# Kernel optimization log

Measured on AMD Instinct MI355X. Metric: run time of the kernel, lower is better.

The kernel has to match this reference:

```python
import math
import jax, jax.numpy as jnp
import numpy as np

EPS = 1e-6
MAX_SCALE_LOG = math.log(100.0)

def rms_norm(x, scale, eps=EPS):
    # x * scale / rms(x), reduction over last dim
    ms = jnp.mean(jnp.square(x), axis=-1, keepdims=True)
    return x * (scale * jax.lax.rsqrt(ms + eps))

def axial_rope_theta(pos, n_heads, d_head, dtype):
    # freqs: linspace in log-space from pi to 10*pi, reshaped to [n_heads, d_head//4]
    f = np.exp(np.linspace(math.log(math.pi), math.log(10.0 * math.pi),
                           n_heads * d_head // 4 + 1)[:-1])
    freqs = jnp.asarray(f.reshape(d_head // 4, n_heads).T, dtype)  # [h, e/4]
    theta_h = pos[:, :, None, 0:1] * freqs  # [n, l, h, e/4]
    theta_w = pos[:, :, None, 1:2] * freqs  # [n, l, h, e/4]
    theta = jnp.concatenate([theta_h, theta_w], axis=-1)  # [n, l, h, e/2]
    return theta.transpose(0, 2, 1, 3)  # [n, h, l, e/2]

def apply_rotary(x, theta):
    d = theta.shape[-1]
    x1, x2, x3 = x[..., :d], x[..., d:2 * d], x[..., 2 * d:]
    cos, sin = jnp.cos(theta), jnp.sin(theta)
    return jnp.concatenate([x1 * cos - x2 * sin, x2 * cos + x1 * sin, x3], axis=-1)

def setup_inputs() -> dict:
    key = jax.random.key(0)
    ks = jax.random.split(key, 8)
    n, l, d_model, d_head = 2, 2048, 1024, 64
    n_heads = d_model // d_head
    x = jax.random.normal(ks[0], (n, l, d_model), jnp.float32)
    pos = jax.random.uniform(ks[1], (n, l, 2), jnp.float32)
    cond = jax.random.normal(ks[2], (n, 1, d_model), jnp.float32)
    # params (torch uses zero-init for w_cond/w_out; small random for a non-degenerate baseline)
    w_cond = jax.random.normal(ks[3], (d_model, d_model), jnp.float32) * 0.02
    w_qkv = jax.random.normal(ks[4], (d_model, 3 * d_model), jnp.float32) * (d_model ** -0.5)
    qk_scale = jnp.full((n_heads,), math.log(10.0), jnp.float32)
    w_out = jax.random.normal(ks[5], (d_model, d_model), jnp.float32) * 0.02
    return {"x": x, "pos": pos, "cond": cond, "w_cond": w_cond,
            "w_qkv": w_qkv, "qk_scale": qk_scale, "w_out": w_out}

def reference(x, pos, cond, w_cond, w_qkv, qk_scale, w_out):
    n, l, d_model = x.shape
    h = qk_scale.shape[0]
    e = d_model // h
    # AdaRMSNorm: scale = linear(cond) + 1
    xn = rms_norm(x, cond @ w_cond + 1.0)
    # QKV projection
    q, k, v = jnp.split(xn @ w_qkv, 3, axis=-1)
    to_heads = lambda t: t.reshape(n, l, h, e).transpose(0, 2, 1, 3)  # [n,h,l,e]
    q, k, v = to_heads(q), to_heads(k), to_heads(v)
    # QKNorm: per-head learned scale, rms over head dim
    s = jnp.exp(0.5 * jnp.minimum(qk_scale, MAX_SCALE_LOG) - 0.25 * math.log(e))
    q = rms_norm(q, s[:, None, None])
    k = rms_norm(k, s[:, None, None])
    # Axial RoPE
    theta = axial_rope_theta(pos, h, e, x.dtype)
    q = apply_rotary(q, theta)
    k = apply_rotary(k, theta)
    # SDPA (no mask)
    attn = jax.nn.softmax(jnp.einsum('nhqe,nhke->nhqk', q, k) / math.sqrt(e), axis=-1)
    o = jnp.einsum('nhqk,nhke->nhqe', attn, v)
    o = o.transpose(0, 2, 1, 3).reshape(n, l, d_model)
    return o @ w_out
```

## Files before the change

kernel.cpp:

```cpp
#include <hip/hip_runtime.h>

typedef unsigned short u16;
typedef unsigned int u32;
typedef short s16x8 __attribute__((ext_vector_type(8)));
typedef short s16x4 __attribute__((ext_vector_type(4)));
typedef float f32x4 __attribute__((ext_vector_type(4)));
typedef float f32x16 __attribute__((ext_vector_type(16)));

#define AS1 __attribute__((address_space(1)))
#define AS3 __attribute__((address_space(3)))

__device__ __forceinline__ float bf2f(u16 u) {
    union { unsigned int i; float f; } x; x.i = ((unsigned int)u) << 16; return x.f;
}
__device__ __forceinline__ u16 f2bf(float f) {
    union { float f; unsigned int i; } x; x.f = f;
    unsigned int r = (x.i + 0x7FFFu + ((x.i >> 16) & 1u)) >> 16;
    return (u16)r;
}
__device__ __forceinline__ void storeOut(u16* p, float v) { *p = f2bf(v); }
__device__ __forceinline__ void storeOut(float* p, float v) { *p = v; }
__device__ __forceinline__ float loadIn(const void* p, size_t i, int isf32) {
    return isf32 ? ((const float*)p)[i] : bf2f(((const u16*)p)[i]);
}
__device__ __forceinline__ float fexp2(float x) {
#if __has_builtin(__builtin_amdgcn_exp2f)
    return __builtin_amdgcn_exp2f(x);
#else
    return exp2f(x);
#endif
}
__device__ __forceinline__ void plswap(u32& a, u32& b) {
#if __has_builtin(__builtin_amdgcn_permlane32_swap)
    const auto r = __builtin_amdgcn_permlane32_swap(a, b, false, false);
    a = (u32)r[0]; b = (u32)r[1];
#else
    asm("v_permlane32_swap_b32 %0, %1" : "+v"(a), "+v"(b));
#endif
}

__global__ __launch_bounds__(256) void detect_dtype(const u16* __restrict__ x,
                                                    int* __restrict__ flag) {
    __shared__ int cnt[4];
    const int tid = threadIdx.x;
    int c = 0;
    #pragma unroll
    for (int i = 0; i < 4; ++i) {
        const u16 u = x[tid * 4 + i];
        const int e = (u >> 7) & 0xFF;
        c += (e >= 101 && e <= 135) ? 1 : 0;
    }
    #pragma unroll
    for (int m = 1; m < 64; m <<= 1) c += __shfl_xor(c, m, 64);
    if ((tid & 63) == 0) cnt[tid >> 6] = c;
    __syncthreads();
    if (tid == 0) {
        const int t = cnt[0] + cnt[1] + cnt[2] + cnt[3];
        *flag = (t < 800) ? 1 : 0;
    }
}

__global__ __launch_bounds__(256) void cond_gemv(const void* __restrict__ cond,
                                                 const void* __restrict__ w,
                                                 float* __restrict__ out,
                                                 const int* __restrict__ flag) {
    const int isf32 = *flag;
    const int d  = blockIdx.x * 256 + threadIdx.x;
    const int n  = blockIdx.y;
    const int k0 = blockIdx.z * 64;
    float acc = 0.f;
    #pragma unroll 8
    for (int k = 0; k < 64; ++k)
        acc += loadIn(cond, n * 1024 + k0 + k, isf32) *
               loadIn(w, (size_t)(k0 + k) * 1024 + d, isf32);
    atomicAdd(out + n * 1024 + d, acc);
}

__global__ __launch_bounds__(256) void rmsnorm_x(const void* __restrict__ x,
                                                 const float* __restrict__ scl,
                                                 u16* __restrict__ xn,
                                                 const int* __restrict__ flag) {
    const int isf32 = *flag;
    const int tok = blockIdx.x;
    const int n = tok >> 11;
    u16* orow = xn + (size_t)tok * 1024;
    const int base = threadIdx.x * 4;
    float f0, f1, f2, f3;
    if (isf32) {
        const float4 v = *(const float4*)((const float*)x + (size_t)tok * 1024 + base);
        f0 = v.x; f1 = v.y; f2 = v.z; f3 = v.w;
    } else {
        s16x4 uv = *(const s16x4*)((const u16*)x + (size_t)tok * 1024 + base);
        f0 = bf2f((u16)uv[0]); f1 = bf2f((u16)uv[1]); f2 = bf2f((u16)uv[2]); f3 = bf2f((u16)uv[3]);
    }
    float ss = f0 * f0 + f1 * f1 + f2 * f2 + f3 * f3;
    #pragma unroll
    for (int m = 1; m < 64; m <<= 1) ss += __shfl_xor(ss, m, 64);
    __shared__ float red[4];
    const int wave = threadIdx.x >> 6, lane = threadIdx.x & 63;
    if (lane == 0) red[wave] = ss;
    __syncthreads();
    float ms = (red[0] + red[1] + red[2] + red[3]) * (1.f / 1024.f);
    float rinv = rsqrtf(ms + 1e-6f);
    orow[base + 0] = f2bf(f0 * (scl[n * 1024 + base + 0] + 1.f) * rinv);
    orow[base + 1] = f2bf(f1 * (scl[n * 1024 + base + 1] + 1.f) * rinv);
    orow[base + 2] = f2bf(f2 * (scl[n * 1024 + base + 2] + 1.f) * rinv);
    orow[base + 3] = f2bf(f3 * (scl[n * 1024 + base + 3] + 1.f) * rinv);
}

__global__ __launch_bounds__(256) void transpose_bf(const void* __restrict__ src,
                                                    u16* __restrict__ dst, int R, int C,
                                                    const int* __restrict__ flag) {
    const int isf32 = *flag;
    __shared__ u16 t[32][33];
    const int c0 = blockIdx.x * 32, r0 = blockIdx.y * 32;
    const int tx = threadIdx.x & 31, ty = threadIdx.x >> 5;
    #pragma unroll
    for (int i = 0; i < 4; ++i)
        t[ty + i * 8][tx] = f2bf(loadIn(src, (size_t)(r0 + ty + i * 8) * C + c0 + tx, isf32));
    __syncthreads();
    #pragma unroll
    for (int i = 0; i < 4; ++i)
        dst[(size_t)(c0 + ty + i * 8) * R + r0 + tx] = t[tx][ty + i * 8];
}

template <typename OutT>
__global__ __launch_bounds__(256) void gemm_bt(const u16* __restrict__ A,
                                               const u16* __restrict__ BT,
                                               OutT* __restrict__ C, int Nn, int K) {
    __shared__ u16 As[128 * 32];
    __shared__ u16 Bs[128 * 32];
    const int tid = threadIdx.x;
    const int wave = tid >> 6, lane = tid & 63;
    const int l15 = lane & 15, quad = lane >> 4;
    const int bm0 = blockIdx.y * 128, bn0 = blockIdx.x * 128;
    const int wr = wave >> 1, wc = wave & 1;
    f32x4 acc[4][4] = {};
    const int srow = lane >> 2;
    const int g = (lane & 3) ^ (srow & 3);
    for (int bk = 0; bk < K; bk += 32) {
        __syncthreads();
        #pragma unroll
        for (int p = 0; p < 2; ++p) {
            const int rowl = p * 64 + wave * 16 + srow;
            const u16* ga = A + (size_t)(bm0 + rowl) * K + bk + g * 8;
            u16* la = As + (p * 64 + wave * 16) * 32;
            __builtin_amdgcn_global_load_lds((const AS1 void*)ga, (AS3 void*)la, 16, 0, 0);
            const u16* gb = BT + (size_t)(bn0 + rowl) * K + bk + g * 8;
            u16* lb = Bs + (p * 64 + wave * 16) * 32;
            __builtin_amdgcn_global_load_lds((const AS1 void*)gb, (AS3 void*)lb, 16, 0, 0);
        }
        __syncthreads();
        s16x8 af[4], bfr[4];
        #pragma unroll
        for (int mt = 0; mt < 4; ++mt) {
            const int r = wr * 64 + mt * 16 + l15;
            af[mt] = *(const s16x8*)(As + r * 32 + ((quad ^ (r & 3)) << 3));
        }
        #pragma unroll
        for (int nt = 0; nt < 4; ++nt) {
            const int r = wc * 64 + nt * 16 + l15;
            bfr[nt] = *(const s16x8*)(Bs + r * 32 + ((quad ^ (r & 3)) << 3));
        }
        #pragma unroll
        for (int mt = 0; mt < 4; ++mt)
            #pragma unroll
            for (int nt = 0; nt < 4; ++nt)
                acc[mt][nt] = __builtin_amdgcn_mfma_f32_16x16x32_bf16(af[mt], bfr[nt], acc[mt][nt], 0, 0, 0);
    }
    #pragma unroll
    for (int mt = 0; mt < 4; ++mt)
        #pragma unroll
        for (int nt = 0; nt < 4; ++nt)
            #pragma unroll
            for (int r = 0; r < 4; ++r) {
                const int row = bm0 + wr * 64 + mt * 16 + quad * 4 + r;
                const int col = bn0 + wc * 64 + nt * 16 + l15;
                storeOut(C + (size_t)row * Nn + col, acc[mt][nt][r]);
            }
}

__global__ __launch_bounds__(256) void qkv_head(const u16* __restrict__ qkv,
                                                const void* __restrict__ pos,
                                                const void* __restrict__ qk_scale,
                                                u16* __restrict__ q_ws,
                                                u16* __restrict__ k_ws,
                                                u16* __restrict__ vtg,
                                                const int* __restrict__ flag) {
    const int isf32 = *flag;
    const int nh = blockIdx.y;
    const int n = nh >> 4, h = nh & 15;
    const int l0 = blockIdx.x * 64;
    const int tid = threadIdx.x;
    const int wave = tid >> 6, lane = tid & 63;

    const float qs = loadIn(qk_scale, h, isf32);
    const float s = __expf(0.5f * fminf(qs, 4.605170186f) - 1.039720771f);
    const float qmul = s * s * 0.125f * 1.44269504089f;
    const int j = lane & 31;
    const float t = (float)((j & 15) * 16 + h);
    const float freq = 3.14159265358979f * __expf(t * (2.302585093f / 256.f));
    const int pj = j >> 4;

    #pragma unroll 2
    for (int it = 0; it < 16; ++it) {
        const int l = l0 + wave * 16 + it;
        const int tok = n * 2048 + l;
        const u16* row = qkv + (size_t)tok * 3072;
        float qv = bf2f(row[h * 64 + lane]);
        float kv = bf2f(row[1024 + h * 64 + lane]);
        float q2 = qv * qv, k2 = kv * kv;
        #pragma unroll
        for (int m = 1; m < 64; m <<= 1) { q2 += __shfl_xor(q2, m, 64); k2 += __shfl_xor(k2, m, 64); }
        float qn = qv * rsqrtf(q2 * (1.f / 64.f) + 1e-6f) * qmul;
        float kn = kv * rsqrtf(k2 * (1.f / 64.f) + 1e-6f);
        const float p = loadIn(pos, tok * 2 + pj, isf32);
        const float th = p * freq;
        const float c = __cosf(th), sn = __sinf(th);
        const float pq = __shfl_xor(qn, 32, 64);
        const float pk = __shfl_xor(kn, 32, 64);
        float qr, kr;
        if (lane < 32) { qr = qn * c - pq * sn; kr = kn * c - pk * sn; }
        else           { qr = qn * c + pq * sn; kr = kn * c + pk * sn; }
        const size_t oidx = ((size_t)nh * 2048 + l) * 64 + lane;
        q_ws[oidx] = f2bf(qr);
        k_ws[oidx] = f2bf(kr);
    }

    __shared__ u16 tbuf[64][65];
    const u16* vsrc = qkv + (size_t)(n * 2048 + l0) * 3072 + 2048 + h * 64;
    #pragma unroll
    for (int it = 0; it < 16; ++it) {
        const int idx = it * 256 + tid;
        const int r = idx >> 6, c = idx & 63;
        tbuf[r][c] = vsrc[(size_t)r * 3072 + c];
    }
    __syncthreads();
    u16* dst = vtg + (size_t)nh * 131072 + l0;
    #pragma unroll
    for (int it = 0; it < 16; ++it) {
        const int idx = it * 256 + tid;
        const int er = idx >> 6, lc = idx & 63;
        dst[(size_t)er * 2048 + lc] = tbuf[lc][er];
    }
}

__global__ __launch_bounds__(1024) void attn10(const u16* __restrict__ Q,
                                               const u16* __restrict__ K,
                                               const u16* __restrict__ Vtg,
                                               u16* __restrict__ O) {
    __shared__ u16 Ks[2][256 * 64];
    __shared__ u16 Vt[2][64 * 256];
    const int nh = blockIdx.y;
    const int q0 = blockIdx.x * 256;
    const int tid = threadIdx.x;
    const int wave = tid >> 6, lane = tid & 63;
    const int wq = wave & 7, ks = wave >> 3;
    const int l31 = lane & 31, h = lane >> 5;
    const size_t hb = (size_t)nh * 2048 * 64;
    const u16* Vbase = Vtg + (size_t)nh * 131072;

    s16x8 qf[4];
    #pragma unroll
    for (int kd = 0; kd < 4; ++kd)
        qf[kd] = *(const s16x8*)(Q + hb + (size_t)(q0 + wq * 32 + l31) * 64 + kd * 16 + h * 8);

    f32x16 Oacc[2] = {};
    float lacc = 0.f;

    auto stage = [&](int ch, int slot) {
        const int kb = ch * 256;
        #pragma unroll
        for (int r = 0; r < 2; ++r) {
            const int row = r * 128 + (tid >> 3);
            const int g = (tid & 7) ^ (row & 7);
            __builtin_amdgcn_global_load_lds(
                (const AS1 void*)(K + hb + (size_t)(kb + row) * 64 + g * 8),
                (AS3 void*)(Ks[slot] + (r * 128 + wave * 8) * 64), 16, 0, 0);
        }
        #pragma unroll
        for (int r = 0; r < 2; ++r) {
            const int er = r * 32 + (tid >> 5);
            const int g2 = (lane & 31) ^ (er & 7);
            __builtin_amdgcn_global_load_lds(
                (const AS1 void*)(Vbase + (size_t)er * 2048 + kb + g2 * 8),
                (AS3 void*)(Vt[slot] + (r * 32 + wave * 2) * 256), 16, 0, 0);
        }
    };

    stage(0, 0);

    for (int j = 0; j < 8; ++j) {
        if (j > 0) __builtin_amdgcn_s_barrier();
        if (j < 7) {
            stage(j + 1, (j + 1) & 1);
            asm volatile("s_waitcnt vmcnt(4)" ::: "memory");
        } else {
            asm volatile("s_waitcnt vmcnt(0)" ::: "memory");
        }
        __builtin_amdgcn_sched_barrier(0);
        __builtin_amdgcn_s_barrier();

        const u16* Kt = Ks[j & 1];
        const u16* Vc = Vt[j & 1];

        #pragma unroll 2
        for (int t = 0; t < 4; ++t) {
            const int kt = ks * 4 + t;
            f32x16 S;
            #pragma unroll
            for (int jj = 0; jj < 16; ++jj) S[jj] = -15.f;
            const int kr = kt * 32 + l31;
            __builtin_amdgcn_s_setprio(1);
            #pragma unroll
            for (int kd = 0; kd < 4; ++kd) {
                const s16x8 kf = *(const s16x8*)(Kt + kr * 64 + ((((kd << 1) + h) ^ (kr & 7)) << 3));
                S = __builtin_amdgcn_mfma_f32_32x32x16_bf16(kf, qf[kd], S, 0, 0, 0);
            }
            __builtin_amdgcn_s_setprio(0);
            float e[16];
            #pragma unroll
            for (int jj = 0; jj < 16; ++jj) e[jj] = fexp2(S[jj]);
            float rs = 0.f;
            #pragma unroll
            for (int jj = 0; jj < 16; ++jj) rs += e[jj];
            lacc += rs;
            u32 c[8];
            #pragma unroll
            for (int jj = 0; jj < 8; ++jj)
                asm("v_cvt_pk_bf16_f32 %0, %1, %2" : "=v"(c[jj]) : "v"(e[2 * jj]), "v"(e[2 * jj + 1]));
            plswap(c[0], c[2]);
            plswap(c[1], c[3]);
            plswap(c[4], c[6]);
            plswap(c[5], c[7]);
            union { u32 u[4]; s16x8 v; } pfa, pfb;
            pfa.u[0] = c[0]; pfa.u[1] = c[1]; pfa.u[2] = c[2]; pfa.u[3] = c[3];
            pfb.u[0] = c[4]; pfb.u[1] = c[5]; pfb.u[2] = c[6]; pfb.u[3] = c[7];
            __builtin_amdgcn_s_setprio(1);
            #pragma unroll
            for (int et = 0; et < 2; ++et) {
                const int er = et * 32 + l31;
                #pragma unroll
                for (int kdp = 0; kdp < 2; ++kdp) {
                    const int ch = kt * 4 + kdp * 2 + h;
                    const s16x8 vf = *(const s16x8*)(Vc + er * 256 + ((ch ^ (er & 7)) << 3));
                    Oacc[et] = __builtin_amdgcn_mfma_f32_32x32x16_bf16(kdp ? pfb.v : pfa.v, vf, Oacc[et], 0, 0, 0);
                }
            }
            __builtin_amdgcn_s_setprio(0);
        }
    }

    __syncthreads();
    float (*Osh)[512] = (float(*)[512]) & Ks[0][0];
    float* Lsh = (float*)&Vt[0][0];
    if (ks == 1) {
        #pragma unroll
        for (int et = 0; et < 2; ++et)
            #pragma unroll
            for (int r = 0; r < 16; ++r)
                Osh[et * 16 + r][wq * 64 + lane] = Oacc[et][r];
        Lsh[wq * 64 + lane] = lacc;
    }
    __syncthreads();
    if (ks == 0) {
        #pragma unroll
        for (int et = 0; et < 2; ++et)
            #pragma unroll
            for (int r = 0; r < 16; ++r)
                Oacc[et][r] += Osh[et * 16 + r][wq * 64 + lane];
        lacc += Lsh[wq * 64 + lane];

        lacc += __shfl_xor(lacc, 32, 64);
        const float linv_l = 1.f / lacc;
        const int n = nh >> 4, hh = nh & 15;
        #pragma unroll
        for (int r = 0; r < 16; ++r) {
            const int ql = (r & 3) + 8 * (r >> 2) + 4 * h;
            const float linv = __shfl(linv_l, ql, 64);
            const int qrow = q0 + wq * 32 + ql;
            #pragma unroll
            for (int et = 0; et < 2; ++et)
                O[((size_t)n * 2048 + qrow) * 1024 + hh * 64 + et * 32 + l31] = f2bf(Oacc[et][r] * linv);
        }
    }
}

extern "C" void kernel_launch(void* const* d_in, const int* in_sizes, int n_in,
                              void* d_out, int out_size, void* d_ws, size_t ws_size,
                              hipStream_t stream) {
    const void* x        = d_in[0];
    const void* pos      = d_in[1];
    const void* cond     = d_in[2];
    const void* w_cond   = d_in[3];
    const void* w_qkv    = d_in[4];
    const void* qk_scale = d_in[5];
    const void* w_out    = d_in[6];

    char* ws = (char*)d_ws;
    constexpr size_t OFS_SCALE = 0;
    constexpr size_t OFS_FLAG  = 8192;
    constexpr size_t OFS_XN    = 16384;
    constexpr size_t OFS_WQKVT = OFS_XN    + 8388608;
    constexpr size_t OFS_WOUTT = OFS_WQKVT + 6291456;
    constexpr size_t OFS_QKV   = OFS_WOUTT + 2097152;
    constexpr size_t OFS_Q     = OFS_QKV   + 25165824;
    constexpr size_t OFS_K     = OFS_Q     + 8388608;
    constexpr size_t OFS_VT    = OFS_K     + 8388608;
    constexpr size_t OFS_O     = OFS_VT    + 8388608;

    float* scale = (float*)(ws + OFS_SCALE);
    int*   flag  = (int*)(ws + OFS_FLAG);
    u16* xn    = (u16*)(ws + OFS_XN);
    u16* wqkvT = (u16*)(ws + OFS_WQKVT);
    u16* woutT = (u16*)(ws + OFS_WOUTT);
    u16* qkv   = (u16*)(ws + OFS_QKV);
    u16* qws   = (u16*)(ws + OFS_Q);
    u16* kws   = (u16*)(ws + OFS_K);
    u16* vtg   = (u16*)(ws + OFS_VT);
    u16* ows   = (u16*)(ws + OFS_O);

    detect_dtype<<<dim3(1), 256, 0, stream>>>((const u16*)x, flag);
    hipMemsetAsync(scale, 0, 2 * 1024 * sizeof(float), stream);
    cond_gemv<<<dim3(4, 2, 16), 256, 0, stream>>>(cond, w_cond, scale, flag);
    rmsnorm_x<<<dim3(4096), 256, 0, stream>>>(x, scale, xn, flag);
    transpose_bf<<<dim3(96, 32), 256, 0, stream>>>(w_qkv, wqkvT, 1024, 3072, flag);
    transpose_bf<<<dim3(32, 32), 256, 0, stream>>>(w_out, woutT, 1024, 1024, flag);
    gemm_bt<u16><<<dim3(24, 32), 256, 0, stream>>>(xn, wqkvT, qkv, 3072, 1024);
    qkv_head<<<dim3(32, 32), 256, 0, stream>>>(qkv, pos, qk_scale, qws, kws, vtg, flag);
    attn10<<<dim3(8, 32), 1024, 0, stream>>>(qws, kws, vtg, ows);
    gemm_bt<float><<<dim3(8, 32), 256, 0, stream>>>(ows, woutT, (float*)d_out, 1024, 1024);
}
```

Baseline: 234.2 us.

## Double-buffer GEMM LDS tiles and vectorize AdaRMSNorm output stores

The GEMM now keeps two LDS slots for the A and B tiles and prefetches the next K-chunk with direct-to-LDS loads while MFMAs run on the current chunk. Explicit vmcnt waits and s_barrier calls replace the two __syncthreads per iteration, so global load latency can overlap with compute. The RMS norm kernel also packs its four bf16 outputs into one vector store instead of four scalar stores. This doubles LDS use per block, which may lower occupancy, and correctness now depends on the hand-written waitcnt counts matching the loads issued.

```diff
diff --git a/kernel.cpp b/kernel.cpp
--- a/kernel.cpp
+++ b/kernel.cpp
@@ -102,10 +102,12 @@
     __syncthreads();
     float ms = (red[0] + red[1] + red[2] + red[3]) * (1.f / 1024.f);
     float rinv = rsqrtf(ms + 1e-6f);
-    orow[base + 0] = f2bf(f0 * (scl[n * 1024 + base + 0] + 1.f) * rinv);
-    orow[base + 1] = f2bf(f1 * (scl[n * 1024 + base + 1] + 1.f) * rinv);
-    orow[base + 2] = f2bf(f2 * (scl[n * 1024 + base + 2] + 1.f) * rinv);
-    orow[base + 3] = f2bf(f3 * (scl[n * 1024 + base + 3] + 1.f) * rinv);
+    s16x4 ov;
+    ov[0] = (short)f2bf(f0 * (scl[n * 1024 + base + 0] + 1.f) * rinv);
+    ov[1] = (short)f2bf(f1 * (scl[n * 1024 + base + 1] + 1.f) * rinv);
+    ov[2] = (short)f2bf(f2 * (scl[n * 1024 + base + 2] + 1.f) * rinv);
+    ov[3] = (short)f2bf(f3 * (scl[n * 1024 + base + 3] + 1.f) * rinv);
+    *(s16x4*)(orow + base) = ov;
 }
 
 __global__ __launch_bounds__(256) void transpose_bf(const void* __restrict__ src,
@@ -128,8 +130,8 @@
 __global__ __launch_bounds__(256) void gemm_bt(const u16* __restrict__ A,
                                                const u16* __restrict__ BT,
                                                OutT* __restrict__ C, int Nn, int K) {
-    __shared__ u16 As[128 * 32];
-    __shared__ u16 Bs[128 * 32];
+    __shared__ u16 As[2][128 * 32];
+    __shared__ u16 Bs[2][128 * 32];
     const int tid = threadIdx.x;
     const int wave = tid >> 6, lane = tid & 63;
     const int l15 = lane & 15, quad = lane >> 4;
@@ -138,29 +140,46 @@
     f32x4 acc[4][4] = {};
     const int srow = lane >> 2;
     const int g = (lane & 3) ^ (srow & 3);
-    for (int bk = 0; bk < K; bk += 32) {
-        __syncthreads();
+
+    auto stageg = [&](int ck, int slot) {
+        const int bk = ck * 32;
         #pragma unroll
         for (int p = 0; p < 2; ++p) {
             const int rowl = p * 64 + wave * 16 + srow;
             const u16* ga = A + (size_t)(bm0 + rowl) * K + bk + g * 8;
-            u16* la = As + (p * 64 + wave * 16) * 32;
+            u16* la = As[slot] + (p * 64 + wave * 16) * 32;
             __builtin_amdgcn_global_load_lds((const AS1 void*)ga, (AS3 void*)la, 16, 0, 0);
             const u16* gb = BT + (size_t)(bn0 + rowl) * K + bk + g * 8;
-            u16* lb = Bs + (p * 64 + wave * 16) * 32;
+            u16* lb = Bs[slot] + (p * 64 + wave * 16) * 32;
             __builtin_amdgcn_global_load_lds((const AS1 void*)gb, (AS3 void*)lb, 16, 0, 0);
         }
-        __syncthreads();
+    };
+
+    const int NC = K >> 5;
+    stageg(0, 0);
+    for (int j = 0; j < NC; ++j) {
+        if (j > 0) __builtin_amdgcn_s_barrier();
+        if (j < NC - 1) {
+            stageg(j + 1, (j + 1) & 1);
+            asm volatile("s_waitcnt vmcnt(4)" ::: "memory");
+        } else {
+            asm volatile("s_waitcnt vmcnt(0)" ::: "memory");
+        }
+        __builtin_amdgcn_sched_barrier(0);
+        __builtin_amdgcn_s_barrier();
+
+        const u16* Ac = As[j & 1];
+        const u16* Bc = Bs[j & 1];
         s16x8 af[4], bfr[4];
         #pragma unroll
         for (int mt = 0; mt < 4; ++mt) {
             const int r = wr * 64 + mt * 16 + l15;
-            af[mt] = *(const s16x8*)(As + r * 32 + ((quad ^ (r & 3)) << 3));
+            af[mt] = *(const s16x8*)(Ac + r * 32 + ((quad ^ (r & 3)) << 3));
         }
         #pragma unroll
         for (int nt = 0; nt < 4; ++nt) {
             const int r = wc * 64 + nt * 16 + l15;
-            bfr[nt] = *(const s16x8*)(Bs + r * 32 + ((quad ^ (r & 3)) << 3));
+            bfr[nt] = *(const s16x8*)(Bc + r * 32 + ((quad ^ (r & 3)) << 3));
         }
         #pragma unroll
         for (int mt = 0; mt < 4; ++mt)
```

Measured after the change: 225.1 us. 1.04x faster.
